# Optimization experiments

Measured on AMD Instinct MI355X. Metric: run time of the kernel, lower is better.

## Reference

```python
import jax, jax.numpy as jnp
import numpy as np

N = 8192
D_IN = 256
D_OUT = 256
E = 131072
P = 2  # number of bottom-to-up hierarchy levels


def gcn_conv(x, edge_index, W, b, num_nodes):
    """PyG-style GCNConv: add self-loops, symmetric normalization, x @ W + b."""
    loops = jnp.arange(num_nodes)
    src = jnp.concatenate([edge_index[0], loops])
    dst = jnp.concatenate([edge_index[1], loops])
    deg = jax.ops.segment_sum(jnp.ones_like(dst, dtype=x.dtype), dst,
                              num_segments=num_nodes)  # [N], >=1 due to self-loops
    dinv = jax.lax.rsqrt(deg)
    norm = dinv[src] * dinv[dst]                         # [E+N]
    h = x @ W                                            # [N, out]
    out = jax.ops.segment_sum(norm[:, None] * h[src], dst, num_segments=num_nodes)
    return out + b


def setup_inputs() -> dict:
    key = jax.random.key(0)
    ks = jax.random.split(key, 8)
    embedding = jax.random.normal(ks[0], (N, D_IN), dtype=jnp.float32)
    down2up_path = jax.random.uniform(ks[1], (P, N, N), dtype=jnp.float32)
    same_level_edge_index = jax.random.randint(ks[2], (2, E), 0, N)
    up2down_edge_index = jax.random.randint(ks[3], (2, E), 0, N)
    W_same = jax.random.normal(ks[4], (D_IN, D_OUT), dtype=jnp.float32) * (1.0 / np.sqrt(D_IN))
    b_same = jnp.zeros((D_OUT,), dtype=jnp.float32)
    W_top = jax.random.normal(ks[5], (D_OUT, D_OUT), dtype=jnp.float32) * (1.0 / np.sqrt(D_OUT))
    b_top = jnp.zeros((D_OUT,), dtype=jnp.float32)
    return {"embedding": embedding, "down2up_path": down2up_path,
            "same_level_edge_index": same_level_edge_index,
            "up2down_edge_index": up2down_edge_index,
            "W_same": W_same, "b_same": b_same,
            "W_top": W_top, "b_top": b_top}


def reference(embedding, down2up_path, same_level_edge_index, up2down_edge_index,
              W_same, b_same, W_top, b_top):
    # ---- bottom_to_up (MEAN path): per-level mm + residual add + row-mean normalize
    emb = embedding
    for p in range(down2up_path.shape[0]):  # small fixed number of hierarchy levels
        A = down2up_path[p]                  # [N, N]
        emb = (emb + A @ emb) * (1.0 / (A.sum(-1) + 1.0))[:, None]
    # ---- same-level GCNConv
    emb = gcn_conv(emb, same_level_edge_index, W_same, b_same, N)
    # ---- top_to_bottom GCNConv
    emb = gcn_conv(emb, up2down_edge_index, W_top, b_top, N)
    return emb
```

## Files before the change

kernel.cpp:

```cpp
#include <hip/hip_runtime.h>
#include <cstdint>

#define NN 8192
#define DD 256

typedef unsigned short u16;
typedef __bf16 bf16x8 __attribute__((ext_vector_type(8)));
typedef float f32x4 __attribute__((ext_vector_type(4)));

__device__ __forceinline__ u16 f2bf(float f) {
    union { float f; unsigned u; } c; c.f = f;
    unsigned u = c.u;
    return (u16)((u + 0x7FFFu + ((u >> 16) & 1u)) >> 16);
}

template<bool AF32, bool ROWSUM, bool ATOMIC>
__global__ __launch_bounds__(256, 2)
void gemm_k(const void* __restrict__ Ap, long ldA,
            const u16* __restrict__ BT, long ldBT,
            float* __restrict__ C, float* __restrict__ rs, int kPer)
{
    __shared__ __align__(16) u16 As[64 * 32];
    __shared__ __align__(16) u16 Bs[256 * 32];

    const int tid  = threadIdx.x;
    const int lane = tid & 63;
    const int wave = tid >> 6;
    const int r    = lane & 15;
    const int q    = lane >> 4;
    const long m0  = (long)blockIdx.x * 64;
    const long k0  = (long)blockIdx.z * kPer;

    f32x4 acc[4][4] = {};
    f32x4 racc[4]   = {};
    bf16x8 ones;
    if constexpr (ROWSUM) {
        union { bf16x8 v; u16 u[8]; } cv;
        u16 pat = (r == 0) ? (u16)0x3F80 : (u16)0;
        #pragma unroll
        for (int j = 0; j < 8; ++j) cv.u[j] = pat;
        ones = cv.v;
    }

    const u16* bBase = BT + (long)(wave * 64 + r) * ldBT + k0 + q * 8;
    const int arow = tid >> 2;
    const int kq8  = tid & 3;
    const float* aBaseF = AF32 ? ((const float*)Ap + (m0 + arow) * ldA + k0 + kq8 * 8) : nullptr;
    const u16* aBaseH = AF32 ? nullptr
                             : ((const u16*)Ap + (m0 + wave * 16 + r) * ldA + k0 + q * 8);
    const int nsteps = kPer >> 5;

    for (int s = 0; s < nsteps; ++s) {
        const long koff = (long)s << 5;
        if constexpr (AF32) {
            const float* ap = aBaseF + koff;
            float4 f0 = *(const float4*)ap;
            float4 f1 = *(const float4*)(ap + 4);
            union { u16 u[8]; uint4 v; } pk;
            pk.u[0] = f2bf(f0.x); pk.u[1] = f2bf(f0.y);
            pk.u[2] = f2bf(f0.z); pk.u[3] = f2bf(f0.w);
            pk.u[4] = f2bf(f1.x); pk.u[5] = f2bf(f1.y);
            pk.u[6] = f2bf(f1.z); pk.u[7] = f2bf(f1.w);
            *(uint4*)(As + (arow >> 4) * 512 + (kq8 * 16 + (arow & 15)) * 8) = pk.v;
        } else {
            __builtin_amdgcn_global_load_lds(
                (const __attribute__((address_space(1))) void*)(aBaseH + koff),
                (__attribute__((address_space(3))) void*)(As + wave * 512 + lane * 8),
                16, 0, 0);
        }
        #pragma unroll
        for (int g2 = 0; g2 < 4; ++g2) {
            __builtin_amdgcn_global_load_lds(
                (const __attribute__((address_space(1))) void*)(bBase + (long)g2 * 16 * ldBT + koff),
                (__attribute__((address_space(3))) void*)(Bs + (wave * 4 + g2) * 512 + lane * 8),
                16, 0, 0);
        }
        __syncthreads();

        bf16x8 af[4], bfr[4];
        #pragma unroll
        for (int i = 0; i < 4; ++i) {
            af[i]  = *(const bf16x8*)(As + i * 512 + lane * 8);
            bfr[i] = *(const bf16x8*)(Bs + (wave * 4 + i) * 512 + lane * 8);
        }
        #pragma unroll
        for (int i = 0; i < 4; ++i)
            #pragma unroll
            for (int j = 0; j < 4; ++j)
                acc[i][j] = __builtin_amdgcn_mfma_f32_16x16x32_bf16(af[i], bfr[j], acc[i][j], 0, 0, 0);
        if constexpr (ROWSUM) {
            if (wave == 0) {
                #pragma unroll
                for (int i = 0; i < 4; ++i)
                    racc[i] = __builtin_amdgcn_mfma_f32_16x16x32_bf16(af[i], ones, racc[i], 0, 0, 0);
            }
        }
        __syncthreads();
    }

    #pragma unroll
    for (int i = 0; i < 4; ++i) {
        const long rowb = m0 + i * 16 + q * 4;
        #pragma unroll
        for (int j = 0; j < 4; ++j) {
            const long col = wave * 64 + j * 16 + r;
            #pragma unroll
            for (int rr2 = 0; rr2 < 4; ++rr2) {
                float v = acc[i][j][rr2];
                float* p = C + (rowb + rr2) * DD + col;
                if constexpr (ATOMIC) atomicAdd(p, v); else *p = v;
            }
        }
        if constexpr (ROWSUM) {
            if (wave == 0 && r == 0) {
                #pragma unroll
                for (int rr2 = 0; rr2 < 4; ++rr2)
                    atomicAdd(rs + rowb + rr2, racc[i][rr2]);
            }
        }
    }
}

__global__ __launch_bounds__(256)
void tc_k(const float* __restrict__ src, u16* __restrict__ dst, int R, int C)
{
    __shared__ u16 t[64][72];
    const int tid = threadIdx.x;
    const int rr = tid >> 2;
    const int cc = (tid & 3) << 4;
    const long r0 = (long)blockIdx.x * 64;
    const long c0 = (long)blockIdx.y * 64;
    const float* sp = src + (r0 + rr) * C + c0 + cc;
    #pragma unroll
    for (int j = 0; j < 16; ++j) t[cc + j][rr] = f2bf(sp[j]);
    __syncthreads();
    u16* dp = dst + (c0 + rr) * (long)R + r0 + cc;
    #pragma unroll
    for (int j = 0; j < 16; ++j) dp[j] = t[rr][cc + j];
}

__global__ __launch_bounds__(256)
void norm0_k(const float* __restrict__ Cacc, const float* __restrict__ rs,
             const float* __restrict__ resid,
             float* __restrict__ outF, u16* __restrict__ outT)
{
    __shared__ u16 t[64][72];
    const int tid = threadIdx.x;
    const int rr = tid >> 2;
    const int cc = (tid & 3) << 4;
    const long i0 = (long)blockIdx.x * 64;
    const int  n0 = blockIdx.y * 64;
    const long i  = i0 + rr;
    const float scale = 1.0f / (rs[i] + 1.0f);
    const float* cp = Cacc + i * DD + n0 + cc;
    const float* rp = resid + i * DD + n0 + cc;
    float* fp = outF + i * DD + n0 + cc;
    #pragma unroll
    for (int j = 0; j < 16; ++j) {
        float v = (rp[j] + cp[j]) * scale;
        fp[j] = v;
        t[cc + j][rr] = f2bf(v);
    }
    __syncthreads();
    u16* op = outT + (long)(n0 + rr) * NN + i0 + cc;
    #pragma unroll
    for (int j = 0; j < 16; ++j) op[j] = t[rr][cc + j];
}

__global__ __launch_bounds__(256)
void norm1_k(const float* __restrict__ Cacc, const float* __restrict__ rs,
             const float* __restrict__ resid, u16* __restrict__ outR)
{
    const long g = ((long)blockIdx.x * 256 + threadIdx.x) * 4;
    const long row = g >> 8;
    const float scale = 1.0f / (rs[row] + 1.0f);
    const float4 c = *(const float4*)(Cacc + g);
    const float4 rv = *(const float4*)(resid + g);
    u16* op = outR + g;
    op[0] = f2bf((rv.x + c.x) * scale);
    op[1] = f2bf((rv.y + c.y) * scale);
    op[2] = f2bf((rv.z + c.z) * scale);
    op[3] = f2bf((rv.w + c.w) * scale);
}

__global__ __launch_bounds__(256)
void count_k(const int* __restrict__ dst, int E, int* __restrict__ counts) {
    int e = blockIdx.x * 256 + threadIdx.x;
    if (e < E) atomicAdd(counts + dst[e], 1);
}

__global__ __launch_bounds__(256)
void scan_k(const int* __restrict__ counts, int* __restrict__ offs,
            int* __restrict__ cursor, float* __restrict__ dinv) {
    __shared__ int sh[256];
    __shared__ int sbase;
    const int tid = threadIdx.x;
    if (tid == 0) sbase = 0;
    __syncthreads();
    for (int base = 0; base < NN; base += 256) {
        int c = counts[base + tid];
        dinv[base + tid] = 1.0f / sqrtf((float)c + 1.0f);
        sh[tid] = c;
        __syncthreads();
        #pragma unroll
        for (int off2 = 1; off2 < 256; off2 <<= 1) {
            int v = (tid >= off2) ? sh[tid - off2] : 0;
            __syncthreads();
            sh[tid] += v;
            __syncthreads();
        }
        int excl = sbase + sh[tid] - c;
        offs[base + tid] = excl;
        cursor[base + tid] = excl;
        int tot = sh[255];
        __syncthreads();
        if (tid == 0) sbase += tot;
        __syncthreads();
    }
    if (tid == 0) offs[NN] = sbase;
}

__global__ __launch_bounds__(256)
void fill_k(const int* __restrict__ src, const int* __restrict__ dst, int E,
            int* __restrict__ cursor, int* __restrict__ csr) {
    int e = blockIdx.x * 256 + threadIdx.x;
    if (e < E) {
        int p = atomicAdd(cursor + dst[e], 1);
        csr[p] = src[e];
    }
}

__global__ __launch_bounds__(256)
void gather_k(const float* __restrict__ h,
              const int* __restrict__ offs,
              const int* __restrict__ csr,
              const float* __restrict__ dinv,
              const float* __restrict__ bias,
              u16* __restrict__ outBF,
              float* __restrict__ outF)
{
    const int node = blockIdx.x * 4 + (threadIdx.x >> 6);
    const int lane = threadIdx.x & 63;
    const float di = dinv[node];
    const float4 hs = ((const float4*)(h + (long)node * DD))[lane];
    const float s0 = di * di;
    float4 acc;
    acc.x = hs.x * s0; acc.y = hs.y * s0; acc.z = hs.z * s0; acc.w = hs.w * s0;

    const int b0 = offs[node], b1 = offs[node + 1];
    for (int e = b0; e < b1; ++e) {
        const int s = csr[e];
        const float w = di * dinv[s];
        const float4 x = ((const float4*)(h + (long)s * DD))[lane];
        acc.x += w * x.x; acc.y += w * x.y; acc.z += w * x.z; acc.w += w * x.w;
    }
    const float4 bv = ((const float4*)bias)[lane];
    acc.x += bv.x; acc.y += bv.y; acc.z += bv.z; acc.w += bv.w;

    if (outF) {
        ((float4*)(outF + (long)node * DD))[lane] = acc;
    } else {
        u16* op = outBF + (long)node * DD + lane * 4;
        op[0] = f2bf(acc.x); op[1] = f2bf(acc.y);
        op[2] = f2bf(acc.z); op[3] = f2bf(acc.w);
    }
}

extern "C" void kernel_launch(void* const* d_in, const int* in_sizes, int n_in,
                              void* d_out, int out_size, void* d_ws, size_t ws_size,
                              hipStream_t stream)
{
    (void)n_in; (void)out_size; (void)ws_size;
    const float* emb0  = (const float*)d_in[0];
    const float* A     = (const float*)d_in[1];
    const int*   eiS   = (const int*)d_in[2];
    const int*   eiU   = (const int*)d_in[3];
    const float* Wsame = (const float*)d_in[4];
    const float* bsame = (const float*)d_in[5];
    const float* Wtop  = (const float*)d_in[6];
    const float* btop  = (const float*)d_in[7];
    const int E = in_sizes[2] / 2;

    char* ws = (char*)d_ws;
    u16*   embT   = (u16*)  (ws + 0);
    float* Cacc   = (float*)(ws + 4194304);
    float* emb1   = (float*)(ws + 12582912);
    u16*   xbf    = (u16*)  (ws + 20971520);
    u16*   WT     = (u16*)  (ws + 25165824);
    float* rsb    = (float*)(ws + 25296896);
    float* dinv   = (float*)(ws + 25329664);
    int*   counts = (int*)  (ws + 25362432);
    int*   offs   = (int*)  (ws + 25395200);
    int*   cursor = (int*)  (ws + 25432064);
    int*   csr    = (int*)  (ws + 25464832);

    const dim3 blk(256);
    const dim3 gDense(128, 1, 4), gGcn(128, 1, 1);
    const dim3 gE((E + 255) / 256), gG(NN / 4);

    tc_k<<<dim3(128, 4), blk, 0, stream>>>(emb0, embT, NN, DD);

    hipMemsetAsync(Cacc, 0, 8388608, stream);
    hipMemsetAsync(rsb, 0, 32768, stream);
    gemm_k<true, true, true><<<gDense, blk, 0, stream>>>(A, NN, embT, NN, Cacc, rsb, 2048);
    norm0_k<<<dim3(128, 4), blk, 0, stream>>>(Cacc, rsb, emb0, emb1, embT);

    hipMemsetAsync(Cacc, 0, 8388608, stream);
    hipMemsetAsync(rsb, 0, 32768, stream);
    gemm_k<true, true, true><<<gDense, blk, 0, stream>>>(A + (size_t)NN * NN, NN, embT, NN, Cacc, rsb, 2048);
    norm1_k<<<dim3(2048), blk, 0, stream>>>(Cacc, rsb, emb1, xbf);

    tc_k<<<dim3(4, 4), blk, 0, stream>>>(Wsame, WT, DD, DD);
    hipMemsetAsync(counts, 0, 32768, stream);
    count_k<<<gE, blk, 0, stream>>>(eiS + E, E, counts);
    scan_k<<<dim3(1), blk, 0, stream>>>(counts, offs, cursor, dinv);
    fill_k<<<gE, blk, 0, stream>>>(eiS, eiS + E, E, cursor, csr);
    gemm_k<false, false, false><<<gGcn, blk, 0, stream>>>(xbf, DD, WT, DD, Cacc, nullptr, 256);
    gather_k<<<gG, blk, 0, stream>>>(Cacc, offs, csr, dinv, bsame, xbf, nullptr);

    tc_k<<<dim3(4, 4), blk, 0, stream>>>(Wtop, WT, DD, DD);
    hipMemsetAsync(counts, 0, 32768, stream);
    count_k<<<gE, blk, 0, stream>>>(eiU + E, E, counts);
    scan_k<<<dim3(1), blk, 0, stream>>>(counts, offs, cursor, dinv);
    fill_k<<<gE, blk, 0, stream>>>(eiU, eiU + E, E, cursor, csr);
    gemm_k<false, false, false><<<gGcn, blk, 0, stream>>>(xbf, DD, WT, DD, Cacc, nullptr, 256);
    gather_k<<<gG, blk, 0, stream>>>(Cacc, offs, csr, dinv, btop, nullptr, (float*)d_out);
}
```

Before: 1.076 ms.

## Replace split-K atomics with per-slice buffers, faster scan, unrolled gather

The dense split-K GEMMs now write each K-slice's partial result and row sums into separate slabs instead of atomically adding into one zeroed buffer, and the normalize kernels sum the four slabs. This drops the memsets and the atomic traffic, but the workspace grows and the normalize passes must read four times more partial data. The A matrix loads become nontemporal, the scan uses wave shuffles with 1024 threads, and the gather loop is unrolled by two to keep more loads in flight.

```diff
diff --git a/kernel.cpp b/kernel.cpp
--- a/kernel.cpp
+++ b/kernel.cpp
@@ -3,6 +3,7 @@
 
 #define NN 8192
 #define DD 256
+#define KS 4
 
 typedef unsigned short u16;
 typedef __bf16 bf16x8 __attribute__((ext_vector_type(8)));
@@ -14,7 +15,7 @@
     return (u16)((u + 0x7FFFu + ((u >> 16) & 1u)) >> 16);
 }
 
-template<bool AF32, bool ROWSUM, bool ATOMIC>
+template<bool AF32, bool ROWSUM>
 __global__ __launch_bounds__(256, 2)
 void gemm_k(const void* __restrict__ Ap, long ldA,
             const u16* __restrict__ BT, long ldBT,
@@ -30,6 +31,7 @@
     const int q    = lane >> 4;
     const long m0  = (long)blockIdx.x * 64;
     const long k0  = (long)blockIdx.z * kPer;
+    float* __restrict__ Cs = C + (long)blockIdx.z * ((long)NN * DD);
 
     f32x4 acc[4][4] = {};
     f32x4 racc[4]   = {};
@@ -54,13 +56,13 @@
         const long koff = (long)s << 5;
         if constexpr (AF32) {
             const float* ap = aBaseF + koff;
-            float4 f0 = *(const float4*)ap;
-            float4 f1 = *(const float4*)(ap + 4);
+            f32x4 f0 = __builtin_nontemporal_load((const f32x4*)ap);
+            f32x4 f1 = __builtin_nontemporal_load((const f32x4*)(ap + 4));
             union { u16 u[8]; uint4 v; } pk;
-            pk.u[0] = f2bf(f0.x); pk.u[1] = f2bf(f0.y);
-            pk.u[2] = f2bf(f0.z); pk.u[3] = f2bf(f0.w);
-            pk.u[4] = f2bf(f1.x); pk.u[5] = f2bf(f1.y);
-            pk.u[6] = f2bf(f1.z); pk.u[7] = f2bf(f1.w);
+            pk.u[0] = f2bf(f0[0]); pk.u[1] = f2bf(f0[1]);
+            pk.u[2] = f2bf(f0[2]); pk.u[3] = f2bf(f0[3]);
+            pk.u[4] = f2bf(f1[0]); pk.u[5] = f2bf(f1[1]);
+            pk.u[6] = f2bf(f1[2]); pk.u[7] = f2bf(f1[3]);
             *(uint4*)(As + (arow >> 4) * 512 + (kq8 * 16 + (arow & 15)) * 8) = pk.v;
         } else {
             __builtin_amdgcn_global_load_lds(
@@ -105,17 +107,14 @@
         for (int j = 0; j < 4; ++j) {
             const long col = wave * 64 + j * 16 + r;
             #pragma unroll
-            for (int rr2 = 0; rr2 < 4; ++rr2) {
-                float v = acc[i][j][rr2];
-                float* p = C + (rowb + rr2) * DD + col;
-                if constexpr (ATOMIC) atomicAdd(p, v); else *p = v;
-            }
+            for (int rr2 = 0; rr2 < 4; ++rr2)
+                Cs[(rowb + rr2) * DD + col] = acc[i][j][rr2];
         }
         if constexpr (ROWSUM) {
             if (wave == 0 && r == 0) {
                 #pragma unroll
                 for (int rr2 = 0; rr2 < 4; ++rr2)
-                    atomicAdd(rs + rowb + rr2, racc[i][rr2]);
+                    rs[(long)blockIdx.z * NN + rowb + rr2] = racc[i][rr2];
             }
         }
     }
@@ -151,13 +150,16 @@
     const long i0 = (long)blockIdx.x * 64;
     const int  n0 = blockIdx.y * 64;
     const long i  = i0 + rr;
-    const float scale = 1.0f / (rs[i] + 1.0f);
-    const float* cp = Cacc + i * DD + n0 + cc;
-    const float* rp = resid + i * DD + n0 + cc;
+    const float rsum = rs[i] + rs[NN + i] + rs[2 * NN + i] + rs[3 * NN + i];
+    const float scale = 1.0f / (rsum + 1.0f);
+    const float* c0p = Cacc + i * DD + n0 + cc;
+    const float* rp  = resid + i * DD + n0 + cc;
     float* fp = outF + i * DD + n0 + cc;
+    const long slab = (long)NN * DD;
     #pragma unroll
     for (int j = 0; j < 16; ++j) {
-        float v = (rp[j] + cp[j]) * scale;
+        float v = rp[j] + c0p[j] + c0p[j + slab] + c0p[j + 2 * slab] + c0p[j + 3 * slab];
+        v *= scale;
         fp[j] = v;
         t[cc + j][rr] = f2bf(v);
     }
@@ -173,14 +175,19 @@
 {
     const long g = ((long)blockIdx.x * 256 + threadIdx.x) * 4;
     const long row = g >> 8;
-    const float scale = 1.0f / (rs[row] + 1.0f);
-    const float4 c = *(const float4*)(Cacc + g);
+    const float rsum = rs[row] + rs[NN + row] + rs[2 * NN + row] + rs[3 * NN + row];
+    const float scale = 1.0f / (rsum + 1.0f);
+    const long slab = (long)NN * DD;
+    const float4 c0 = *(const float4*)(Cacc + g);
+    const float4 c1 = *(const float4*)(Cacc + g + slab);
+    const float4 c2 = *(const float4*)(Cacc + g + 2 * slab);
+    const float4 c3 = *(const float4*)(Cacc + g + 3 * slab);
     const float4 rv = *(const float4*)(resid + g);
     u16* op = outR + g;
-    op[0] = f2bf((rv.x + c.x) * scale);
-    op[1] = f2bf((rv.y + c.y) * scale);
-    op[2] = f2bf((rv.z + c.z) * scale);
-    op[3] = f2bf((rv.w + c.w) * scale);
+    op[0] = f2bf((rv.x + c0.x + c1.x + c2.x + c3.x) * scale);
+    op[1] = f2bf((rv.y + c0.y + c1.y + c2.y + c3.y) * scale);
+    op[2] = f2bf((rv.z + c0.z + c1.z + c2.z + c3.z) * scale);
+    op[3] = f2bf((rv.w + c0.w + c1.w + c2.w + c3.w) * scale);
 }
 
 __global__ __launch_bounds__(256)
@@ -189,33 +196,42 @@
     if (e < E) atomicAdd(counts + dst[e], 1);
 }
 
-__global__ __launch_bounds__(256)
+__global__ __launch_bounds__(1024)
 void scan_k(const int* __restrict__ counts, int* __restrict__ offs,
             int* __restrict__ cursor, float* __restrict__ dinv) {
-    __shared__ int sh[256];
+    __shared__ int wpre[17];
     __shared__ int sbase;
-    const int tid = threadIdx.x;
-    if (tid == 0) sbase = 0;
+    const int tid  = threadIdx.x;
+    const int lane = tid & 63;
+    const int wid  = tid >> 6;
+    if (tid == 0) { sbase = 0; wpre[0] = 0; }
     __syncthreads();
-    for (int base = 0; base < NN; base += 256) {
-        int c = counts[base + tid];
+    for (int base = 0; base < NN; base += 1024) {
+        const int c = counts[base + tid];
         dinv[base + tid] = 1.0f / sqrtf((float)c + 1.0f);
-        sh[tid] = c;
-        __syncthreads();
-        #pragma unroll
-        for (int off2 = 1; off2 < 256; off2 <<= 1) {
-            int v = (tid >= off2) ? sh[tid - off2] : 0;
-            __syncthreads();
-            sh[tid] += v;
-            __syncthreads();
-        }
-        int excl = sbase + sh[tid] - c;
-        offs[base + tid] = excl;
+        int x = c;
+        #pragma unroll
+        for (int d = 1; d < 64; d <<= 1) {
+            int y = __shfl_up(x, d, 64);
+            if (lane >= d) x += y;
+        }
+        if (lane == 63) wpre[wid + 1] = x;
+        __syncthreads();
+        if (wid == 0) {
+            int w = (lane < 16) ? wpre[lane + 1] : 0;
+            #pragma unroll
+            for (int d = 1; d < 16; d <<= 1) {
+                int y = __shfl_up(w, d, 64);
+                if (lane >= d) w += y;
+            }
+            if (lane < 16) wpre[lane + 1] = w;
+        }
+        __syncthreads();
+        const int excl = sbase + wpre[wid] + (x - c);
+        offs[base + tid]   = excl;
         cursor[base + tid] = excl;
-        int tot = sh[255];
-        __syncthreads();
-        if (tid == 0) sbase += tot;
-        __syncthreads();
+        __syncthreads();
+        if (tid == 0) sbase += wpre[16];
     }
     if (tid == 0) offs[NN] = sbase;
 }
@@ -248,7 +264,19 @@
     acc.x = hs.x * s0; acc.y = hs.y * s0; acc.z = hs.z * s0; acc.w = hs.w * s0;
 
     const int b0 = offs[node], b1 = offs[node + 1];
-    for (int e = b0; e < b1; ++e) {
+    int e = b0;
+    for (; e + 2 <= b1; e += 2) {
+        const int sa = csr[e], sb = csr[e + 1];
+        const float wa = di * dinv[sa];
+        const float wb = di * dinv[sb];
+        const float4 xa = ((const float4*)(h + (long)sa * DD))[lane];
+        const float4 xb = ((const float4*)(h + (long)sb * DD))[lane];
+        acc.x += wa * xa.x + wb * xb.x;
+        acc.y += wa * xa.y + wb * xb.y;
+        acc.z += wa * xa.z + wb * xb.z;
+        acc.w += wa * xa.w + wb * xb.w;
+    }
+    if (e < b1) {
         const int s = csr[e];
         const float w = di * dinv[s];
         const float4 x = ((const float4*)(h + (long)s * DD))[lane];
@@ -284,45 +312,41 @@
     char* ws = (char*)d_ws;
     u16*   embT   = (u16*)  (ws + 0);
     float* Cacc   = (float*)(ws + 4194304);
-    float* emb1   = (float*)(ws + 12582912);
-    u16*   xbf    = (u16*)  (ws + 20971520);
-    u16*   WT     = (u16*)  (ws + 25165824);
-    float* rsb    = (float*)(ws + 25296896);
-    float* dinv   = (float*)(ws + 25329664);
-    int*   counts = (int*)  (ws + 25362432);
-    int*   offs   = (int*)  (ws + 25395200);
-    int*   cursor = (int*)  (ws + 25432064);
-    int*   csr    = (int*)  (ws + 25464832);
+    float* emb1   = (float*)(ws + 37748736);
+    u16*   xbf    = (u16*)  (ws + 46137344);
+    u16*   WT     = (u16*)  (ws + 50331648);
+    float* rsb    = (float*)(ws + 50462720);
+    float* dinv   = (float*)(ws + 50593792);
+    int*   counts = (int*)  (ws + 50626560);
+    int*   offs   = (int*)  (ws + 50659328);
+    int*   cursor = (int*)  (ws + 50696192);
+    int*   csr    = (int*)  (ws + 50728960);
 
     const dim3 blk(256);
-    const dim3 gDense(128, 1, 4), gGcn(128, 1, 1);
+    const dim3 gDense(128, 1, KS), gGcn(128, 1, 1);
     const dim3 gE((E + 255) / 256), gG(NN / 4);
 
     tc_k<<<dim3(128, 4), blk, 0, stream>>>(emb0, embT, NN, DD);
 
-    hipMemsetAsync(Cacc, 0, 8388608, stream);
-    hipMemsetAsync(rsb, 0, 32768, stream);
-    gemm_k<true, true, true><<<gDense, blk, 0, stream>>>(A, NN, embT, NN, Cacc, rsb, 2048);
+    gemm_k<true, true><<<gDense, blk, 0, stream>>>(A, NN, embT, NN, Cacc, rsb, NN / KS);
     norm0_k<<<dim3(128, 4), blk, 0, stream>>>(Cacc, rsb, emb0, emb1, embT);
 
-    hipMemsetAsync(Cacc, 0, 8388608, stream);
-    hipMemsetAsync(rsb, 0, 32768, stream);
-    gemm_k<true, true, true><<<gDense, blk, 0, stream>>>(A + (size_t)NN * NN, NN, embT, NN, Cacc, rsb, 2048);
+    gemm_k<true, true><<<gDense, blk, 0, stream>>>(A + (size_t)NN * NN, NN, embT, NN, Cacc, rsb, NN / KS);
     norm1_k<<<dim3(2048), blk, 0, stream>>>(Cacc, rsb, emb1, xbf);
 
     tc_k<<<dim3(4, 4), blk, 0, stream>>>(Wsame, WT, DD, DD);
     hipMemsetAsync(counts, 0, 32768, stream);
     count_k<<<gE, blk, 0, stream>>>(eiS + E, E, counts);
-    scan_k<<<dim3(1), blk, 0, stream>>>(counts, offs, cursor, dinv);
+    scan_k<<<dim3(1), dim3(1024), 0, stream>>>(counts, offs, cursor, dinv);
     fill_k<<<gE, blk, 0, stream>>>(eiS, eiS + E, E, cursor, csr);
-    gemm_k<false, false, false><<<gGcn, blk, 0, stream>>>(xbf, DD, WT, DD, Cacc, nullptr, 256);
+    gemm_k<false, false><<<gGcn, blk, 0, stream>>>(xbf, DD, WT, DD, Cacc, nullptr, 256);
     gather_k<<<gG, blk, 0, stream>>>(Cacc, offs, csr, dinv, bsame, xbf, nullptr);
 
     tc_k<<<dim3(4, 4), blk, 0, stream>>>(Wtop, WT, DD, DD);
     hipMemsetAsync(counts, 0, 32768, stream);
     count_k<<<gE, blk, 0, stream>>>(eiU + E, E, counts);
-    scan_k<<<dim3(1), blk, 0, stream>>>(counts, offs, cursor, dinv);
+    scan_k<<<dim3(1), dim3(1024), 0, stream>>>(counts, offs, cursor, dinv);
     fill_k<<<gE, blk, 0, stream>>>(eiU, eiU + E, E, cursor, csr);
-    gemm_k<false, false, false><<<gGcn, blk, 0, stream>>>(xbf, DD, WT, DD, Cacc, nullptr, 256);
+    gemm_k<false, false><<<gGcn, blk, 0, stream>>>(xbf, DD, WT, DD, Cacc, nullptr, 256);
     gather_k<<<gG, blk, 0, stream>>>(Cacc, offs, csr, dinv, btop, nullptr, (float*)d_out);
 }
```

Result: faster. 991.7 us (-7.8%).
